# Kernel tuning notes

Measured on AMD Instinct MI355X. Metric: run time of the kernel, lower is better.

Reference implementation:

```python
import jax, jax.numpy as jnp
import numpy as np

LN_EPS = 1e-5


def _layernorm(x, g, b):
    m = jnp.mean(x, axis=-1, keepdims=True)
    v = jnp.mean((x - m) ** 2, axis=-1, keepdims=True)
    return (x - m) * jax.lax.rsqrt(v + LN_EPS) * g + b


def _gcn_conv(x, row, col, ew, W, b):
    # linear projection
    x = x @ W + b  # [N, out]
    n = x.shape[0]
    # weighted degree per source node (index_add over row)
    deg = jax.ops.segment_sum(ew, row, num_segments=n)  # [N]
    safe = jnp.where(deg > 0, deg, 1.0)
    dis = jnp.where(deg > 0, jax.lax.rsqrt(safe), 0.0)  # deg^-0.5, inf -> 0
    norm = dis[row] * ew * dis[col]  # [E]
    # gather-scale-scatter aggregation
    return jax.ops.segment_sum(norm[:, None] * x[col], row, num_segments=n)


def setup_inputs() -> dict:
    key = jax.random.key(0)
    ks = jax.random.split(key, 8)
    N, E, D_IN, D_H, D_OUT = 50000, 800000, 384, 256, 128
    x = jax.random.normal(ks[0], (N, D_IN), dtype=jnp.float32)
    edge_index = jax.random.randint(ks[1], (2, E), 0, N, dtype=jnp.int64)
    edge_weight = jax.random.uniform(ks[2], (E,), dtype=jnp.float32)
    W1 = jax.random.normal(ks[3], (D_IN, D_H), dtype=jnp.float32) * 0.02
    b1 = jnp.zeros((D_H,), dtype=jnp.float32)
    W2 = jax.random.normal(ks[4], (D_H, D_OUT), dtype=jnp.float32) * 0.02
    b2 = jnp.zeros((D_OUT,), dtype=jnp.float32)
    g1 = jnp.ones((D_H,), dtype=jnp.float32)
    be1 = jnp.zeros((D_H,), dtype=jnp.float32)
    g2 = jnp.ones((D_OUT,), dtype=jnp.float32)
    be2 = jnp.zeros((D_OUT,), dtype=jnp.float32)
    return {"x": x, "edge_index": edge_index, "edge_weight": edge_weight,
            "W1": W1, "b1": b1, "W2": W2, "b2": b2,
            "g1": g1, "be1": be1, "g2": g2, "be2": be2}


def reference(x, edge_index, edge_weight, W1, b1, W2, b2, g1, be1, g2, be2):
    row, col = edge_index[0], edge_index[1]
    h = _gcn_conv(x, row, col, edge_weight, W1, b1)
    h = _layernorm(h, g1, be1)
    h = jax.nn.relu(h)
    # dropout is identity in eval mode
    h = _gcn_conv(h, row, col, edge_weight, W2, b2)
    h = _layernorm(h, g2, be2)
    return h
```

## Files before the change

kernel.cpp:

```cpp
#include <hip/hip_runtime.h>


constexpr float LN_EPS = 1e-5f;
constexpr int   SLOTS  = 64;

typedef __attribute__((ext_vector_type(8))) short short8;
typedef __attribute__((ext_vector_type(4))) float f32x4;
typedef __attribute__((ext_vector_type(2))) float f32x2;

static __device__ __forceinline__ unsigned short f2bf(float f) {
    unsigned u = __float_as_uint(f);
    u += 0x7FFFu + ((u >> 16) & 1u);
    return (unsigned short)(u >> 16);
}
static __device__ __forceinline__ float bf2f(unsigned short h) {
    return __uint_as_float(((unsigned)h) << 16);
}
static __device__ __forceinline__ short8 f2bf8(float4 a, float4 b) {
    short8 r;
    r[0] = (short)f2bf(a.x); r[1] = (short)f2bf(a.y);
    r[2] = (short)f2bf(a.z); r[3] = (short)f2bf(a.w);
    r[4] = (short)f2bf(b.x); r[5] = (short)f2bf(b.y);
    r[6] = (short)f2bf(b.z); r[7] = (short)f2bf(b.w);
    return r;
}

#if defined(__has_builtin)
#if __has_builtin(__builtin_amdgcn_global_load_lds)
#define HAS_GLL 1
#endif
#endif

#ifdef HAS_GLL
static __device__ __forceinline__ void gll16(const void* g, void* l) {
    __builtin_amdgcn_global_load_lds(
        (__attribute__((address_space(1))) void*)g,
        (__attribute__((address_space(3))) void*)l, 16, 0, 0);
}
#endif

static __device__ __forceinline__ int swz(int r) {
    return (r & 3) ^ ((r >> 2) & 3);
}

__global__ __launch_bounds__(256) void k_pre(
    const int* __restrict__ row, const int* __restrict__ col,
    const float* __restrict__ ew, int* __restrict__ cnt,
    unsigned* __restrict__ edges4, int E, int histBlocks,
    const float* __restrict__ W1, const float* __restrict__ W2,
    unsigned short* __restrict__ W1P, unsigned short* __restrict__ W2P)
{
    constexpr int K1 = 384, N1 = 256, K2 = 256, N2 = 128;
    constexpr int WTB = (K1 * N1 + K2 * N2) / 256;

    const int bx = blockIdx.x;
    const int m2 = 2 * (histBlocks < WTB ? histBlocks : WTB);
    bool isHist;
    int  id;
    if (bx < m2) { isHist = !(bx & 1); id = bx >> 1; }
    else {
        id = (m2 >> 1) + (bx - m2);
        isHist = histBlocks > WTB;
    }

    if (isHist) {
        int e = id * 256 + threadIdx.x;
        if (e >= E) return;
        int r = row[e];
        int o = atomicAdd(cnt + r, 1);
        if (o < SLOTS)
            edges4[(size_t)r * SLOTS + o] =
                ((unsigned)col[e] << 16) | (unsigned)f2bf(ew[e]);
    } else {
        int o = id * 256 + threadIdx.x;
        if (o < K1 * N1) {
            int cc = o & 31, n = (o >> 5) % N1, p = o / (N1 * 32);
            int c = cc >> 3, j = cc & 7;
            int k = p * 32 + (((c ^ swz(n & 15)) & 3) << 3) + j;
            W1P[o] = f2bf(W1[(size_t)k * N1 + n]);
        } else {
            int o2 = o - K1 * N1;
            int cc = o2 & 31, n = (o2 >> 5) % N2, p = o2 / (N2 * 32);
            int c = cc >> 3, j = cc & 7;
            int k = p * 32 + (((c ^ swz(n & 15)) & 3) << 3) + j;
            W2P[o2] = f2bf(W2[(size_t)k * N2 + n]);
        }
    }
}

__global__ __launch_bounds__(256) void k_dis(
    const int* __restrict__ cnt, const unsigned* __restrict__ edges4,
    float* __restrict__ dis, int n)
{
    const int gw   = (blockIdx.x * 256 + threadIdx.x) >> 6;
    const int lane = threadIdx.x & 63;
    if (gw >= n) return;
    int c = cnt[gw]; if (c > SLOTS) c = SLOTS;
    float v = 0.0f;
    if (lane < c)
        v = bf2f((unsigned short)(edges4[(size_t)gw * SLOTS + lane] & 0xffffu));
    #pragma unroll
    for (int off = 32; off; off >>= 1) v += __shfl_xor(v, off);
    if (lane == 0) dis[gw] = v > 0.0f ? rsqrtf(v) : 0.0f;
}

template<bool AF32, int NFULL, int K>
__global__ __launch_bounds__(256, 4) void k_gemm_mfma(
    const void* __restrict__ Av, const unsigned short* __restrict__ BP,
    const float* __restrict__ bias, unsigned short* __restrict__ C, int M)
{
    constexpr int BM = 64, BN = 128, BK = 32;
    constexpr int MR = 4, NF = 2;
    constexpr int AB = BM * BK * 2;
    constexpr int BB = BN * BK * 2;
    constexpr int TB = AB + BB;

    __shared__ char smem[2 * TB];

    const int t    = threadIdx.x;
    const int lane = t & 63;
    const int wid  = t >> 6;
    const int row0 = blockIdx.x * BM;
    const int col0 = blockIdx.y * BN;
    const int fr   = lane & 15;
    const int fq   = lane >> 4;
    const int nbw  = wid * 32;
    const int nt   = K / BK;

    const int cOff = ((fq ^ swz(fr)) & 3) << 3;

    const float*          Af = (const float*)Av;
    const unsigned short* Ab = (const unsigned short*)Av;

    f32x4 acc[MR][NF] = {};

    auto srcA = [&](int slot, int k0) -> const void* {
        int ra = slot >> 2, ca = slot & 3;
        int gr = row0 + ra; if (gr >= M) gr = M - 1;
        return (const void*)(Ab + (size_t)gr * K + k0 + ca * 8);
    };
    auto srcB = [&](int slot, int st) -> const void* {
        int rb = slot >> 2, cb = slot & 3;
        return (const void*)(BP + ((size_t)st * NFULL + col0 + rb) * 32 + cb * 8);
    };
    auto ldA32 = [&](int st, short8& rv) {
        int ra = t >> 2, ca = t & 3;
        int cs = ca ^ (swz(ra & 15) & 3);
        int gr = row0 + ra; if (gr >= M) gr = M - 1;
        const float* p = Af + (size_t)gr * K + st * BK + cs * 8;
        rv = f2bf8(*(const float4*)p, *(const float4*)(p + 4));
    };

    auto compute = [&](char* buf) {
        const unsigned short* As = (const unsigned short*)buf;
        const unsigned short* Bs = (const unsigned short*)(buf + AB);
        short8 af[MR], bfr[NF];
        #pragma unroll
        for (int i = 0; i < MR; ++i)
            af[i] = *(const short8*)(As + (i * 16 + fr) * 32 + cOff);
        #pragma unroll
        for (int j = 0; j < NF; ++j)
            bfr[j] = *(const short8*)(Bs + (nbw + j * 16 + fr) * 32 + cOff);
        #pragma unroll
        for (int i = 0; i < MR; ++i)
            #pragma unroll
            for (int j = 0; j < NF; ++j)
                acc[i][j] = __builtin_amdgcn_mfma_f32_16x16x32_bf16(
                    af[i], bfr[j], acc[i][j], 0, 0, 0);
    };

#ifdef HAS_GLL
    if constexpr (AF32) {
        auto gllB = [&](int buf, int st) {
            char* Bs = smem + buf * TB + AB;
            gll16(srcB(t, st), Bs + t * 16);
            gll16(srcB(256 + t, st), Bs + (256 + t) * 16);
        };
        short8 a0;
        ldA32(0, a0);
        gllB(0, 0);
        __syncthreads();
        *(short8*)(smem + t * 16) = a0;
        __syncthreads();
        int cur = 0;
        for (int st = 0; st < nt; ++st) {
            short8 an;
            if (st + 1 < nt) { ldA32(st + 1, an); gllB(cur ^ 1, st + 1); }
            compute(smem + cur * TB);
            __syncthreads();
            if (st + 1 < nt)
                *(short8*)(smem + (cur ^ 1) * TB + t * 16) = an;
            __syncthreads();
            cur ^= 1;
        }
    } else {
        auto stage = [&](int buf, int st) {
            char* As = smem + buf * TB;
            char* Bs = As + AB;
            gll16(srcA(t, st * BK), As + t * 16);
            gll16(srcB(t, st), Bs + t * 16);
            gll16(srcB(256 + t, st), Bs + (256 + t) * 16);
        };
        stage(0, 0);
        __syncthreads();
        int cur = 0;
        for (int st = 0; st < nt; ++st) {
            if (st + 1 < nt) stage(cur ^ 1, st + 1);
            compute(smem + cur * TB);
            __syncthreads();
            cur ^= 1;
        }
    }
#else
    for (int st = 0; st < nt; ++st) {
        short8 ar;
        if constexpr (AF32) ldA32(st, ar);
        else                ar = *(const short8*)srcA(t, st * BK);
        int4 b0 = *(const int4*)srcB(t, st);
        int4 b1 = *(const int4*)srcB(256 + t, st);
        __syncthreads();
        *(short8*)(smem + t * 16) = ar;
        *(int4*)(smem + AB + t * 16) = b0;
        *(int4*)(smem + AB + (256 + t) * 16) = b1;
        __syncthreads();
        compute(smem);
    }
#endif

    #pragma unroll
    for (int i = 0; i < MR; ++i) {
        #pragma unroll
        for (int j = 0; j < NF; ++j) {
            const int c = col0 + nbw + j * 16 + fr;
            const float bvv = bias[c];
            #pragma unroll
            for (int r = 0; r < 4; ++r) {
                const int rr = row0 + i * 16 + fq * 4 + r;
                if (rr < M)
                    C[(size_t)rr * NFULL + c] = f2bf(acc[i][j][r] + bvv);
            }
        }
    }
}

template<int D, bool RELU, bool OUTBF, bool SWZ>
__global__ __launch_bounds__(256) void k_agg_ln(
    const unsigned short* __restrict__ feat, const int* __restrict__ cnt,
    const unsigned* __restrict__ edges4, const float* __restrict__ dis,
    const float* __restrict__ g, const float* __restrict__ b,
    void* __restrict__ outv, int n)
{
    constexpr int EV  = 16;
    constexpr int LPR = D / EV;
    constexpr int EPI = 64 / LPR;
    const int gw   = (blockIdx.x * 256 + threadIdx.x) >> 6;
    const int lane = threadIdx.x & 63;
    if (gw >= n) return;

    const int sub = lane / LPR;
    const int el  = (lane % LPR) * EV;

    int j1 = cnt[gw]; if (j1 > SLOTS) j1 = SLOTS;
    const unsigned* eb = edges4 + (size_t)gw * SLOTS;
    const float disr = dis[gw];

    f32x2 acc[8] = {};

    unsigned e0 = (sub < j1)       ? eb[sub]       : 0u;
    unsigned e1 = (EPI + sub < j1) ? eb[EPI + sub] : 0u;
    float dc0 = dis[e0 >> 16];
    uint4 u0, u1;
    {
        const unsigned short* p = feat + (size_t)(e0 >> 16) * D + el;
        u0 = *(const uint4*)p;
        u1 = *(const uint4*)(p + 8);
    }

    for (int j = 0; j < j1; j += EPI) {
        unsigned e2 = (j + 2 * EPI + sub < j1) ? eb[j + 2 * EPI + sub] : 0u;
        float dc1 = dis[e1 >> 16];
        const unsigned short* p = feat + (size_t)(e1 >> 16) * D + el;
        uint4 v0 = *(const uint4*)p;
        uint4 v1 = *(const uint4*)(p + 8);

        const float wv = bf2f((unsigned short)(e0 & 0xffffu)) * dc0;
        const unsigned a[8] = {u0.x, u0.y, u0.z, u0.w, u1.x, u1.y, u1.z, u1.w};
        #pragma unroll
        for (int i = 0; i < 8; ++i) {
            f32x2 h;
            h.x = __uint_as_float(a[i] << 16);
            h.y = __uint_as_float(a[i] & 0xffff0000u);
            acc[i] += h * wv;
        }
        u0 = v0; u1 = v1; e0 = e1; e1 = e2; dc0 = dc1;
    }

    #pragma unroll
    for (int off = LPR; off < 64; off <<= 1)
        #pragma unroll
        for (int i = 0; i < 8; ++i) {
            acc[i].x += __shfl_xor(acc[i].x, off);
            acc[i].y += __shfl_xor(acc[i].y, off);
        }

    #pragma unroll
    for (int i = 0; i < 8; ++i) acc[i] *= disr;

    float s = 0.0f;
    #pragma unroll
    for (int i = 0; i < 8; ++i) s += acc[i].x + acc[i].y;
    #pragma unroll
    for (int off = 32; off; off >>= 1) s += __shfl_xor(s, off);
    const float m = s * (1.0f / (EPI * D));

    float q = 0.0f;
    #pragma unroll
    for (int i = 0; i < 8; ++i) {
        float dx = acc[i].x - m, dy = acc[i].y - m;
        q += dx * dx + dy * dy;
    }
    #pragma unroll
    for (int off = 32; off; off >>= 1) q += __shfl_xor(q, off);
    const float r = rsqrtf(q * (1.0f / (EPI * D)) + LN_EPS);

    if (lane < LPR) {
        float o[16];
        #pragma unroll
        for (int i = 0; i < 4; ++i) {
            float4 gv = *(const float4*)(g + el + i * 4);
            float4 bv = *(const float4*)(b + el + i * 4);
            const float vals[4] = {acc[2 * i].x, acc[2 * i].y,
                                   acc[2 * i + 1].x, acc[2 * i + 1].y};
            const float gg[4] = {gv.x, gv.y, gv.z, gv.w};
            const float bb[4] = {bv.x, bv.y, bv.z, bv.w};
            #pragma unroll
            for (int k2 = 0; k2 < 4; ++k2) {
                float tv = (vals[k2] - m) * r * gg[k2] + bb[k2];
                if constexpr (RELU) tv = fmaxf(tv, 0.0f);
                o[i * 4 + k2] = tv;
            }
        }
        if constexpr (OUTBF) {
            short8 lo, hi;
            #pragma unroll
            for (int i = 0; i < 8; ++i) {
                lo[i] = (short)f2bf(o[i]);
                hi[i] = (short)f2bf(o[8 + i]);
            }
            unsigned short* ob = (unsigned short*)outv + (size_t)gw * D;
            const int w0 = el & ~31;
            const int c0 = (el >> 3) & 3;
            const int sA = SWZ ? swz(gw & 15) : 0;
            *(short8*)(ob + w0 + (((c0 ^ sA) & 3) << 3))       = lo;
            *(short8*)(ob + w0 + ((((c0 + 1) ^ sA) & 3) << 3)) = hi;
        } else {
            float* op = (float*)outv + (size_t)gw * D + el;
            *(float4*)(op)      = make_float4(o[0],  o[1],  o[2],  o[3]);
            *(float4*)(op + 4)  = make_float4(o[4],  o[5],  o[6],  o[7]);
            *(float4*)(op + 8)  = make_float4(o[8],  o[9],  o[10], o[11]);
            *(float4*)(op + 12) = make_float4(o[12], o[13], o[14], o[15]);
        }
    }
}

extern "C" void kernel_launch(void* const* d_in, const int* in_sizes, int n_in,
                              void* d_out, int out_size, void* d_ws, size_t ws_size,
                              hipStream_t stream)
{
    (void)n_in; (void)out_size; (void)ws_size;

    constexpr int DIN = 384, DH = 256, DOUT = 128;

    const float* x   = (const float*)d_in[0];
    const int*   ei  = (const int*)  d_in[1];
    const float* ew  = (const float*)d_in[2];
    const float* W1  = (const float*)d_in[3];
    const float* b1  = (const float*)d_in[4];
    const float* W2  = (const float*)d_in[5];
    const float* b2  = (const float*)d_in[6];
    const float* g1  = (const float*)d_in[7];
    const float* be1 = (const float*)d_in[8];
    const float* g2  = (const float*)d_in[9];
    const float* be2 = (const float*)d_in[10];
    float* out = (float*)d_out;

    const int N = in_sizes[0] / DIN;
    const int E = in_sizes[2];
    const int* row = ei;
    const int* col = ei + E;

    char* w = (char*)d_ws;
    auto carve = [&](size_t bytes) {
        char* p = w;
        w += (bytes + 255) & ~(size_t)255;
        return p;
    };
    int*            cnt    = (int*)     carve((size_t)N * 4);
    float*          dis    = (float*)   carve((size_t)N * 4);
    unsigned*       edges4 = (unsigned*)carve((size_t)N * SLOTS * 4);
    unsigned short* W1P    = (unsigned short*)carve((size_t)DIN * DH * 2);
    unsigned short* W2P    = (unsigned short*)carve((size_t)DH * DOUT * 2);
    unsigned short* h1     = (unsigned short*)carve((size_t)N * DH * 2);
    unsigned short* h1ln   = (unsigned short*)carve((size_t)N * DH * 2);
    unsigned short* h2     = (unsigned short*)carve((size_t)N * DOUT * 2);

    const int gE = (E + 255) / 256;
    const int gW = (N + 3) / 4;
    const int gG = (N + 63) / 64;
    constexpr int WTB = (DIN * DH + DH * DOUT) / 256;

    hipMemsetAsync(cnt, 0, (size_t)N * 4, stream);
    k_pre<<<gE + WTB, 256, 0, stream>>>(
        row, col, ew, cnt, edges4, E, gE, W1, W2, W1P, W2P);
    k_dis<<<gW, 256, 0, stream>>>(cnt, edges4, dis, N);

    {
        dim3 grid(gG, DH / 128);
        k_gemm_mfma<true, DH, DIN><<<grid, 256, 0, stream>>>(x, W1P, b1, h1, N);
    }
    k_agg_ln<DH, true, true, true><<<gW, 256, 0, stream>>>(
        h1, cnt, edges4, dis, g1, be1, h1ln, N);

    {
        dim3 grid(gG, DOUT / 128);
        k_gemm_mfma<false, DOUT, DH><<<grid, 256, 0, stream>>>(h1ln, W2P, b2, h2, N);
    }
    k_agg_ln<DOUT, false, false, false><<<gW, 256, 0, stream>>>(
        h2, cnt, edges4, dis, g2, be2, out, N);
}
```

Before: 212.3 us.

## Fuse edge histogram bucketing into first GEMM kernel launch; split weight pack

The edge bucketing (atomic per-row slot fill) now runs in the same launch as the first layer's MFMA GEMM, with blocks interleaved between histogram and GEMM roles. Weight packing moves to its own small kernel that runs first, because the GEMM needs the packed weights. The goal is to overlap the atomic-bound scatter with the compute-bound GEMM and to drop one separate launch. In exchange, histogram blocks share the GEMM kernel's LDS and register budget, which could lower their occupancy.

Result: faster. 192.3 us (-9.5%).

```diff
diff --git a/kernel.cpp b/kernel.cpp
--- a/kernel.cpp
+++ b/kernel.cpp
@@ -43,24 +43,53 @@
     return (r & 3) ^ ((r >> 2) & 3);
 }
 
-__global__ __launch_bounds__(256) void k_pre(
-    const int* __restrict__ row, const int* __restrict__ col,
-    const float* __restrict__ ew, int* __restrict__ cnt,
-    unsigned* __restrict__ edges4, int E, int histBlocks,
+__global__ __launch_bounds__(256) void k_wt(
     const float* __restrict__ W1, const float* __restrict__ W2,
     unsigned short* __restrict__ W1P, unsigned short* __restrict__ W2P)
 {
     constexpr int K1 = 384, N1 = 256, K2 = 256, N2 = 128;
-    constexpr int WTB = (K1 * N1 + K2 * N2) / 256;
+    int o = blockIdx.x * 256 + threadIdx.x;
+    if (o < K1 * N1) {
+        int cc = o & 31, n = (o >> 5) % N1, p = o / (N1 * 32);
+        int c = cc >> 3, j = cc & 7;
+        int k = p * 32 + (((c ^ swz(n & 15)) & 3) << 3) + j;
+        W1P[o] = f2bf(W1[(size_t)k * N1 + n]);
+    } else {
+        int o2 = o - K1 * N1;
+        if (o2 < K2 * N2) {
+            int cc = o2 & 31, n = (o2 >> 5) % N2, p = o2 / (N2 * 32);
+            int c = cc >> 3, j = cc & 7;
+            int k = p * 32 + (((c ^ swz(n & 15)) & 3) << 3) + j;
+            W2P[o2] = f2bf(W2[(size_t)k * N2 + n]);
+        }
+    }
+}
+
+__global__ __launch_bounds__(256, 4) void k_g1h(
+    const float* __restrict__ Af, const unsigned short* __restrict__ BP,
+    const float* __restrict__ bias, unsigned short* __restrict__ C, int M,
+    const int* __restrict__ row, const int* __restrict__ colv,
+    const float* __restrict__ ew, int* __restrict__ cnt,
+    unsigned* __restrict__ edges4, int E, int histBlocks, int gemmBlocks)
+{
+    constexpr int NFULL = 256, K = 384;
+    constexpr int BM = 64, BN = 128, BK = 32;
+    constexpr int MR = 4, NF = 2;
+    constexpr int AB = BM * BK * 2;
+    constexpr int BB = BN * BK * 2;
+    constexpr int TB = AB + BB;
+
+    __shared__ char smem[2 * TB];
 
     const int bx = blockIdx.x;
-    const int m2 = 2 * (histBlocks < WTB ? histBlocks : WTB);
+    const int mn = histBlocks < gemmBlocks ? histBlocks : gemmBlocks;
+    const int m2 = 2 * mn;
     bool isHist;
     int  id;
     if (bx < m2) { isHist = !(bx & 1); id = bx >> 1; }
     else {
-        id = (m2 >> 1) + (bx - m2);
-        isHist = histBlocks > WTB;
+        id = mn + (bx - m2);
+        isHist = histBlocks > gemmBlocks;
     }
 
     if (isHist) {
@@ -70,20 +99,104 @@
         int o = atomicAdd(cnt + r, 1);
         if (o < SLOTS)
             edges4[(size_t)r * SLOTS + o] =
-                ((unsigned)col[e] << 16) | (unsigned)f2bf(ew[e]);
-    } else {
-        int o = id * 256 + threadIdx.x;
-        if (o < K1 * N1) {
-            int cc = o & 31, n = (o >> 5) % N1, p = o / (N1 * 32);
-            int c = cc >> 3, j = cc & 7;
-            int k = p * 32 + (((c ^ swz(n & 15)) & 3) << 3) + j;
-            W1P[o] = f2bf(W1[(size_t)k * N1 + n]);
-        } else {
-            int o2 = o - K1 * N1;
-            int cc = o2 & 31, n = (o2 >> 5) % N2, p = o2 / (N2 * 32);
-            int c = cc >> 3, j = cc & 7;
-            int k = p * 32 + (((c ^ swz(n & 15)) & 3) << 3) + j;
-            W2P[o2] = f2bf(W2[(size_t)k * N2 + n]);
+                ((unsigned)colv[e] << 16) | (unsigned)f2bf(ew[e]);
+        return;
+    }
+
+    const int t    = threadIdx.x;
+    const int lane = t & 63;
+    const int wid  = t >> 6;
+    const int row0 = (id >> 1) * BM;
+    const int col0 = (id & 1) * BN;
+    const int fr   = lane & 15;
+    const int fq   = lane >> 4;
+    const int nbw  = wid * 32;
+    const int nt   = K / BK;
+
+    const int cOff = ((fq ^ swz(fr)) & 3) << 3;
+
+    f32x4 acc[MR][NF] = {};
+
+    auto srcB = [&](int slot, int st) -> const void* {
+        int rb = slot >> 2, cb = slot & 3;
+        return (const void*)(BP + ((size_t)st * NFULL + col0 + rb) * 32 + cb * 8);
+    };
+    auto ldA32 = [&](int st, short8& rv) {
+        int ra = t >> 2, ca = t & 3;
+        int cs = ca ^ (swz(ra & 15) & 3);
+        int gr = row0 + ra; if (gr >= M) gr = M - 1;
+        const float* p = Af + (size_t)gr * K + st * BK + cs * 8;
+        rv = f2bf8(*(const float4*)p, *(const float4*)(p + 4));
+    };
+
+    auto compute = [&](char* buf) {
+        const unsigned short* As = (const unsigned short*)buf;
+        const unsigned short* Bs = (const unsigned short*)(buf + AB);
+        short8 af[MR], bfr[NF];
+        #pragma unroll
+        for (int i = 0; i < MR; ++i)
+            af[i] = *(const short8*)(As + (i * 16 + fr) * 32 + cOff);
+        #pragma unroll
+        for (int j = 0; j < NF; ++j)
+            bfr[j] = *(const short8*)(Bs + (nbw + j * 16 + fr) * 32 + cOff);
+        #pragma unroll
+        for (int i = 0; i < MR; ++i)
+            #pragma unroll
+            for (int j = 0; j < NF; ++j)
+                acc[i][j] = __builtin_amdgcn_mfma_f32_16x16x32_bf16(
+                    af[i], bfr[j], acc[i][j], 0, 0, 0);
+    };
+
+#ifdef HAS_GLL
+    auto gllB = [&](int buf, int st) {
+        char* Bs = smem + buf * TB + AB;
+        gll16(srcB(t, st), Bs + t * 16);
+        gll16(srcB(256 + t, st), Bs + (256 + t) * 16);
+    };
+    short8 a0;
+    ldA32(0, a0);
+    gllB(0, 0);
+    __syncthreads();
+    *(short8*)(smem + t * 16) = a0;
+    __syncthreads();
+    int cur = 0;
+    for (int st = 0; st < nt; ++st) {
+        short8 an;
+        if (st + 1 < nt) { ldA32(st + 1, an); gllB(cur ^ 1, st + 1); }
+        compute(smem + cur * TB);
+        __syncthreads();
+        if (st + 1 < nt)
+            *(short8*)(smem + (cur ^ 1) * TB + t * 16) = an;
+        __syncthreads();
+        cur ^= 1;
+    }
+#else
+    for (int st = 0; st < nt; ++st) {
+        short8 ar;
+        ldA32(st, ar);
+        int4 b0 = *(const int4*)srcB(t, st);
+        int4 b1 = *(const int4*)srcB(256 + t, st);
+        __syncthreads();
+        *(short8*)(smem + t * 16) = ar;
+        *(int4*)(smem + AB + t * 16) = b0;
+        *(int4*)(smem + AB + (256 + t) * 16) = b1;
+        __syncthreads();
+        compute(smem);
+    }
+#endif
+
+    #pragma unroll
+    for (int i = 0; i < MR; ++i) {
+        #pragma unroll
+        for (int j = 0; j < NF; ++j) {
+            const int c = col0 + nbw + j * 16 + fr;
+            const float bvv = bias[c];
+            #pragma unroll
+            for (int r = 0; r < 4; ++r) {
+                const int rr = row0 + i * 16 + fq * 4 + r;
+                if (rr < M)
+                    C[(size_t)rr * NFULL + c] = f2bf(acc[i][j][r] + bvv);
+            }
         }
     }
 }
@@ -104,9 +217,9 @@
     if (lane == 0) dis[gw] = v > 0.0f ? rsqrtf(v) : 0.0f;
 }
 
-template<bool AF32, int NFULL, int K>
+template<int NFULL, int K>
 __global__ __launch_bounds__(256, 4) void k_gemm_mfma(
-    const void* __restrict__ Av, const unsigned short* __restrict__ BP,
+    const unsigned short* __restrict__ A, const unsigned short* __restrict__ BP,
     const float* __restrict__ bias, unsigned short* __restrict__ C, int M)
 {
     constexpr int BM = 64, BN = 128, BK = 32;
@@ -129,26 +242,16 @@
 
     const int cOff = ((fq ^ swz(fr)) & 3) << 3;
 
-    const float*          Af = (const float*)Av;
-    const unsigned short* Ab = (const unsigned short*)Av;
-
     f32x4 acc[MR][NF] = {};
 
     auto srcA = [&](int slot, int k0) -> const void* {
         int ra = slot >> 2, ca = slot & 3;
         int gr = row0 + ra; if (gr >= M) gr = M - 1;
-        return (const void*)(Ab + (size_t)gr * K + k0 + ca * 8);
+        return (const void*)(A + (size_t)gr * K + k0 + ca * 8);
     };
     auto srcB = [&](int slot, int st) -> const void* {
         int rb = slot >> 2, cb = slot & 3;
         return (const void*)(BP + ((size_t)st * NFULL + col0 + rb) * 32 + cb * 8);
-    };
-    auto ldA32 = [&](int st, short8& rv) {
-        int ra = t >> 2, ca = t & 3;
-        int cs = ca ^ (swz(ra & 15) & 3);
-        int gr = row0 + ra; if (gr >= M) gr = M - 1;
-        const float* p = Af + (size_t)gr * K + st * BK + cs * 8;
-        rv = f2bf8(*(const float4*)p, *(const float4*)(p + 4));
     };
 
     auto compute = [&](char* buf) {
@@ -170,56 +273,29 @@
     };
 
 #ifdef HAS_GLL
-    if constexpr (AF32) {
-        auto gllB = [&](int buf, int st) {
-            char* Bs = smem + buf * TB + AB;
-            gll16(srcB(t, st), Bs + t * 16);
-            gll16(srcB(256 + t, st), Bs + (256 + t) * 16);
-        };
-        short8 a0;
-        ldA32(0, a0);
-        gllB(0, 0);
-        __syncthreads();
-        *(short8*)(smem + t * 16) = a0;
-        __syncthreads();
-        int cur = 0;
-        for (int st = 0; st < nt; ++st) {
-            short8 an;
-            if (st + 1 < nt) { ldA32(st + 1, an); gllB(cur ^ 1, st + 1); }
-            compute(smem + cur * TB);
-            __syncthreads();
-            if (st + 1 < nt)
-                *(short8*)(smem + (cur ^ 1) * TB + t * 16) = an;
-            __syncthreads();
-            cur ^= 1;
-        }
-    } else {
-        auto stage = [&](int buf, int st) {
-            char* As = smem + buf * TB;
-            char* Bs = As + AB;
-            gll16(srcA(t, st * BK), As + t * 16);
-            gll16(srcB(t, st), Bs + t * 16);
-            gll16(srcB(256 + t, st), Bs + (256 + t) * 16);
-        };
-        stage(0, 0);
-        __syncthreads();
-        int cur = 0;
-        for (int st = 0; st < nt; ++st) {
-            if (st + 1 < nt) stage(cur ^ 1, st + 1);
-            compute(smem + cur * TB);
-            __syncthreads();
-            cur ^= 1;
-        }
+    auto stage = [&](int buf, int st) {
+        char* As = smem + buf * TB;
+        char* Bs = As + AB;
+        gll16(srcA(t, st * BK), As + t * 16);
+        gll16(srcB(t, st), Bs + t * 16);
+        gll16(srcB(256 + t, st), Bs + (256 + t) * 16);
+    };
+    stage(0, 0);
+    __syncthreads();
+    int cur = 0;
+    for (int st = 0; st < nt; ++st) {
+        if (st + 1 < nt) stage(cur ^ 1, st + 1);
+        compute(smem + cur * TB);
+        __syncthreads();
+        cur ^= 1;
     }
 #else
     for (int st = 0; st < nt; ++st) {
-        short8 ar;
-        if constexpr (AF32) ldA32(st, ar);
-        else                ar = *(const short8*)srcA(t, st * BK);
+        int4 ar = *(const int4*)srcA(t, st * BK);
         int4 b0 = *(const int4*)srcB(t, st);
         int4 b1 = *(const int4*)srcB(256 + t, st);
         __syncthreads();
-        *(short8*)(smem + t * 16) = ar;
+        *(int4*)(smem + t * 16) = ar;
         *(int4*)(smem + AB + t * 16) = b0;
         *(int4*)(smem + AB + (256 + t) * 16) = b1;
         __syncthreads();
@@ -407,23 +483,21 @@
     const int gE = (E + 255) / 256;
     const int gW = (N + 3) / 4;
     const int gG = (N + 63) / 64;
+    const int gemmB = gG * (DH / 128);
     constexpr int WTB = (DIN * DH + DH * DOUT) / 256;
 
     hipMemsetAsync(cnt, 0, (size_t)N * 4, stream);
-    k_pre<<<gE + WTB, 256, 0, stream>>>(
-        row, col, ew, cnt, edges4, E, gE, W1, W2, W1P, W2P);
+    k_wt<<<WTB, 256, 0, stream>>>(W1, W2, W1P, W2P);
+    k_g1h<<<gE + gemmB, 256, 0, stream>>>(
+        x, W1P, b1, h1, N, row, col, ew, cnt, edges4, E, gE, gemmB);
     k_dis<<<gW, 256, 0, stream>>>(cnt, edges4, dis, N);
 
-    {
-        dim3 grid(gG, DH / 128);
-        k_gemm_mfma<true, DH, DIN><<<grid, 256, 0, stream>>>(x, W1P, b1, h1, N);
-    }
     k_agg_ln<DH, true, true, true><<<gW, 256, 0, stream>>>(
         h1, cnt, edges4, dis, g1, be1, h1ln, N);
 
     {
         dim3 grid(gG, DOUT / 128);
-        k_gemm_mfma<false, DOUT, DH><<<grid, 256, 0, stream>>>(h1ln, W2P, b2, h2, N);
+        k_gemm_mfma<DOUT, DH><<<grid, 256, 0, stream>>>(h1ln, W2P, b2, h2, N);
     }
     k_agg_ln<DOUT, false, false, false><<<gW, 256, 0, stream>>>(
         h2, cnt, edges4, dis, g2, be2, out, N);
```
